# Kernel tuning notes

Measured on AMD Instinct MI355X. Metric: run time of the kernel, lower is better.

Reference implementation:

```python
import jax, jax.numpy as jnp
import numpy as np
from math import sqrt


def setup_inputs() -> dict:
    key = jax.random.key(0)
    ks = jax.random.split(key, 10)
    N, C = 192, 96  # C = N // 2
    n, h, w = 8, 64, 64
    s = lambda fan_in: 1.0 / np.sqrt(fan_in)
    return {
        "x": jax.random.normal(ks[0], (n, N, h, w), dtype=jnp.float32),
        "pe": jax.random.normal(ks[1], (N, 120, 120), dtype=jnp.float32) * 0.02,
        "wq": jax.random.normal(ks[2], (C, N), dtype=jnp.float32) * s(N),
        "bq": jax.random.normal(ks[3], (C,), dtype=jnp.float32) * 0.01,
        "wk": jax.random.normal(ks[4], (C, N), dtype=jnp.float32) * s(N),
        "bk": jax.random.normal(ks[5], (C,), dtype=jnp.float32) * 0.01,
        "wv": jax.random.normal(ks[6], (C, N), dtype=jnp.float32) * s(N),
        "bv": jax.random.normal(ks[7], (C,), dtype=jnp.float32) * 0.01,
        "wz": jax.random.normal(ks[8], (N, C), dtype=jnp.float32) * s(C),
        "bz": jax.random.normal(ks[9], (N,), dtype=jnp.float32) * 0.01,
    }


def _conv1x1(x, w, b):
    # x: [n, cin, h, w]; w: [cout, cin]; b: [cout]
    return jnp.einsum("oc,nchw->nohw", w, x) + b[None, :, None, None]


def reference(x, pe, wq, bq, wk, bk, wv, bv, wz, bz):
    n, c_in, h, w = x.shape
    hw = h * w
    # 2D positional encoding, sliced to the actual spatial size
    x = x + pe[None, :, :h, :w]
    c = wq.shape[0]  # N // 2
    q = _conv1x1(x, wq, bq).reshape(n, c, hw)   # [n, c, hw]
    k = _conv1x1(x, wk, bk).reshape(n, c, hw)   # [n, c, hw]
    v = _conv1x1(x, wv, bv).reshape(n, c, hw)   # [n, c, hw]
    scale = sqrt(hw)
    # logits[n, i, j] = sum_c q[n,c,i] * k[n,c,j]
    logits = jnp.einsum("nci,ncj->nij", q, k) / scale  # [n, hw, hw]
    weights = jax.nn.softmax(logits, axis=-1)
    # z[n, c, i] = sum_j weights[n,i,j] * v[n,c,j]
    z = jnp.einsum("nij,ncj->nci", weights, v).reshape(n, c, h, w)
    z = _conv1x1(z, wz, bz)  # [n, N, h, w]
    return x + z
```

## Files before the change

kernel.cpp:

```cpp
#include <hip/hip_runtime.h>
#include <hip/hip_bf16.h>

#define HW 4096
#define CIN 192
#define CMID 96

typedef __attribute__((ext_vector_type(8))) short bf16x8;
typedef __attribute__((ext_vector_type(4))) float f32x4;
typedef __attribute__((ext_vector_type(16))) float f32x16;
typedef __attribute__((ext_vector_type(4))) unsigned int u32x4;

static __device__ __forceinline__ unsigned short f2bf(float f) {
    union { float f; unsigned int u; } v;
    v.f = f;
    unsigned int r = v.u + 0x7fffu + ((v.u >> 16) & 1u);
    return (unsigned short)(r >> 16);
}
static __device__ __forceinline__ float b2f(unsigned short h) {
    union { unsigned int u; float f; } v;
    v.u = ((unsigned int)h) << 16;
    return v.f;
}

static __device__ __forceinline__ void gload16(const void* g, void* l) {
    __builtin_amdgcn_global_load_lds(
        (const __attribute__((address_space(1))) unsigned int*)g,
        (__attribute__((address_space(3))) unsigned int*)l, 16, 0, 0);
}

#define SCQ (0.015625f * 1.44269504089f)

__global__ __launch_bounds__(256) void convw_kernel(
    const float* __restrict__ wq, const float* __restrict__ wk,
    const float* __restrict__ wv, const float* __restrict__ wz,
    unsigned short* __restrict__ wqkvb, unsigned short* __restrict__ wzb)
{
    int idx = blockIdx.x * 256 + threadIdx.x;
    if (idx < 3 * CMID * CIN) {
        int m = idx / (CMID * CIN), r = idx % (CMID * CIN);
        const float* w = (m == 0) ? wq : ((m == 1) ? wk : wv);
        wqkvb[idx] = f2bf(w[r]);
    } else if (idx < 3 * CMID * CIN + CIN * CMID) {
        int r = idx - 3 * CMID * CIN;
        wzb[r] = f2bf(wz[r]);
    }
}

__global__ __launch_bounds__(256) void qkv_kernel(
    const float* __restrict__ x, const float* __restrict__ pe,
    const unsigned short* __restrict__ wqkvb,
    const float* __restrict__ bq, const float* __restrict__ bk,
    const float* __restrict__ bv,
    unsigned short* __restrict__ Q, unsigned short* __restrict__ K,
    unsigned short* __restrict__ V)
{
    const int n = blockIdx.y, i0 = blockIdx.x * 64, t = threadIdx.x;
    __shared__ unsigned short xt[64 * 200];

    for (int idx = t; idx < CIN * 64; idx += 256) {
        int c = idx >> 6, il = idx & 63;
        float v = x[((size_t)n * CIN + c) * HW + i0 + il]
                + pe[c * 14400 + blockIdx.x * 120 + il];
        xt[il * 200 + c] = f2bf(v);
    }
    __syncthreads();

    const int w = t >> 6, lane = t & 63, l15 = lane & 15, lg = lane >> 4;
    const int p0 = w * 16;

    bf16x8 af[6];
    #pragma unroll
    for (int f = 0; f < 6; ++f)
        af[f] = *(const bf16x8*)(xt + (p0 + l15) * 200 + f * 32 + lg * 8);

    #pragma unroll
    for (int ct = 0; ct < 18; ++ct) {
        const int m = ct / 6, c6 = ct % 6;
        f32x4 acc = (f32x4){0.f, 0.f, 0.f, 0.f};
        const unsigned short* wrow = wqkvb + (ct * 16 + l15) * CIN + lg * 8;
        #pragma unroll
        for (int f = 0; f < 6; ++f) {
            bf16x8 wf = *(const bf16x8*)(wrow + f * 32);
            if (m < 2)
                acc = __builtin_amdgcn_mfma_f32_16x16x32_bf16(wf, af[f], acc, 0, 0, 0);
            else
                acc = __builtin_amdgcn_mfma_f32_16x16x32_bf16(af[f], wf, acc, 0, 0, 0);
        }
        if (m < 2) {
            f32x4 bv4 = *(const f32x4*)(((m == 0) ? bq : bk) + c6 * 16 + lg * 4);
            ushort4 pk4;
            if (m == 0) {
                pk4.x = f2bf((acc[0] + bv4[0]) * SCQ);
                pk4.y = f2bf((acc[1] + bv4[1]) * SCQ);
                pk4.z = f2bf((acc[2] + bv4[2]) * SCQ);
                pk4.w = f2bf((acc[3] + bv4[3]) * SCQ);
            } else {
                pk4.x = f2bf(acc[0] + bv4[0]);
                pk4.y = f2bf(acc[1] + bv4[1]);
                pk4.z = f2bf(acc[2] + bv4[2]);
                pk4.w = f2bf(acc[3] + bv4[3]);
            }
            unsigned short* dst = ((m == 0) ? Q : K) + (size_t)n * HW * CMID;
            *(ushort4*)(dst + (size_t)(i0 + p0 + l15) * CMID + c6 * 16 + lg * 4) = pk4;
        } else {
            const float bias = bv[c6 * 16 + l15];
            ushort4 pk4;
            pk4.x = f2bf(acc[0] + bias); pk4.y = f2bf(acc[1] + bias);
            pk4.z = f2bf(acc[2] + bias); pk4.w = f2bf(acc[3] + bias);
            *(ushort4*)(V + (size_t)n * CMID * HW + (size_t)(c6 * 16 + l15) * HW
                          + i0 + p0 + lg * 4) = pk4;
        }
    }
}

__global__ __launch_bounds__(256, 2) void attn_kernel(
    const unsigned short* __restrict__ Q, const unsigned short* __restrict__ K,
    const unsigned short* __restrict__ V,
    unsigned short* __restrict__ zp, float* __restrict__ lp)
{
    const int bid = blockIdx.x;
    const int n    = bid & 7;
    const int iblk = (bid >> 3) & 15;
    const int js   = bid >> 7;

    const int t = threadIdx.x, w = t >> 6, lane = t & 63;
    const int l31 = lane & 31, hi = lane >> 5;
    const int ib = iblk * 256 + w * 64;

    __shared__ unsigned short Ks[3][32 * 128];
    __shared__ unsigned short Vs[2][96 * 64];

    const unsigned short* Qb = Q + (size_t)n * HW * CMID;
    const unsigned short* Kb = K + (size_t)n * HW * CMID;
    const unsigned short* Vb = V + (size_t)n * CMID * HW;

    bf16x8 qf[2][6];
    #pragma unroll
    for (int is = 0; is < 2; ++is)
        #pragma unroll
        for (int kc = 0; kc < 6; ++kc)
            qf[is][kc] = *(const bf16x8*)(Qb + (size_t)(ib + is * 32 + l31) * CMID
                                            + kc * 16 + hi * 8);

    int ksoff[2], vsoff[3];
    #pragma unroll
    for (int s = 0; s < 2; ++s) {
        int row = 8 * w + 4 * s + (lane >> 4);
        ksoff[s] = row * CMID + (((lane & 15) ^ (row & 7)) * 8);
    }
    #pragma unroll
    for (int s = 0; s < 3; ++s) {
        int c = 8 * (w * 3 + s) + (lane >> 3);
        vsoff[s] = c * HW + (((lane & 7) ^ (c & 7)) * 8);
    }

    const int j00 = js * 1024;

#define STAGE_K(TILE, KB) do {                                                 \
    _Pragma("unroll") for (int s = 0; s < 2; ++s)                              \
        gload16(Kb + (size_t)(j00 + (TILE) * 32) * CMID + ksoff[s],            \
                &Ks[KB][(w * 2 + s) * 512]);                                   \
} while (0)
#define STAGE_V(WND, VB) do {                                                  \
    _Pragma("unroll") for (int s = 0; s < 3; ++s)                              \
        gload16(Vb + (size_t)(j00 + (WND) * 64) + vsoff[s],                    \
                &Vs[VB][(w * 3 + s) * 512]);                                   \
} while (0)

    f32x16 O[2][3];
    #pragma unroll
    for (int is = 0; is < 2; ++is)
        #pragma unroll
        for (int cc = 0; cc < 3; ++cc)
            #pragma unroll
            for (int e = 0; e < 16; ++e) O[is][cc][e] = 0.f;
    float lsum0 = 0.f, lsum1 = 0.f;

    STAGE_K(0, 0);
    STAGE_K(1, 1);
    STAGE_V(0, 0);
    asm volatile("s_waitcnt vmcnt(0)" ::: "memory");
    __builtin_amdgcn_s_barrier();

#define BODY(KBUF, VBUF, VHALF) do {                                           \
    const unsigned short* Kc = &Ks[KBUF][0];                                   \
    const unsigned short* Vc = &Vs[VBUF][0];                                   \
    f32x16 s0, s1;                                                             \
    _Pragma("unroll") for (int e = 0; e < 16; ++e) { s0[e] = 0.f; s1[e] = 0.f; } \
    __builtin_amdgcn_s_setprio(1);                                             \
    _Pragma("unroll") for (int kc = 0; kc < 6; ++kc) {                         \
        bf16x8 kf = *(const bf16x8*)(Kc + l31 * 128 +                          \
                      (((kc * 2 + hi) ^ (l31 & 7)) << 3));                     \
        s0 = __builtin_amdgcn_mfma_f32_32x32x16_bf16(kf, qf[0][kc], s0, 0, 0, 0); \
        s1 = __builtin_amdgcn_mfma_f32_32x32x16_bf16(kf, qf[1][kc], s1, 0, 0, 0); \
    }                                                                          \
    __builtin_amdgcn_s_setprio(0);                                             \
    unsigned pkk[2][4][2];                                                     \
    _Pragma("unroll") for (int q = 0; q < 4; ++q)                              \
        _Pragma("unroll") for (int rp = 0; rp < 2; ++rp) {                     \
            float lo0 = __builtin_exp2f(s0[q * 4 + 2 * rp]);                   \
            float hh0 = __builtin_exp2f(s0[q * 4 + 2 * rp + 1]);               \
            float lo1 = __builtin_exp2f(s1[q * 4 + 2 * rp]);                   \
            float hh1 = __builtin_exp2f(s1[q * 4 + 2 * rp + 1]);               \
            lsum0 += lo0 + hh0; lsum1 += lo1 + hh1;                            \
            asm("v_cvt_pk_bf16_f32 %0, %1, %2"                                 \
                : "=v"(pkk[0][q][rp]) : "v"(lo0), "v"(hh0));                   \
            asm("v_cvt_pk_bf16_f32 %0, %1, %2"                                 \
                : "=v"(pkk[1][q][rp]) : "v"(lo1), "v"(hh1));                   \
        }                                                                      \
    u32x4 pfu[2][2];                                                           \
    _Pragma("unroll") for (int is = 0; is < 2; ++is)                           \
        _Pragma("unroll") for (int jc = 0; jc < 2; ++jc) {                     \
            unsigned x0 = pkk[is][2 * jc][0], y0 = pkk[is][2 * jc + 1][0];     \
            unsigned x1 = pkk[is][2 * jc][1], y1 = pkk[is][2 * jc + 1][1];     \
            asm("v_permlane32_swap_b32 %0, %1" : "+v"(y0), "+v"(x0));          \
            asm("v_permlane32_swap_b32 %0, %1" : "+v"(y1), "+v"(x1));          \
            pfu[is][jc][0] = x0; pfu[is][jc][1] = x1;                          \
            pfu[is][jc][2] = y0; pfu[is][jc][3] = y1;                          \
        }                                                                      \
    __builtin_amdgcn_s_setprio(1);                                             \
    _Pragma("unroll") for (int jc = 0; jc < 2; ++jc) {                         \
        bf16x8 pa0 = __builtin_bit_cast(bf16x8, pfu[0][jc]);                   \
        bf16x8 pa1 = __builtin_bit_cast(bf16x8, pfu[1][jc]);                   \
        _Pragma("unroll") for (int cc = 0; cc < 3; ++cc) {                     \
            bf16x8 vf = *(const bf16x8*)(Vc + (cc * 32 + l31) * 64 +           \
                          ((((VHALF) * 4 + jc * 2 + hi) ^ (l31 & 7)) << 3));   \
            O[0][cc] = __builtin_amdgcn_mfma_f32_32x32x16_bf16(pa0, vf, O[0][cc], 0, 0, 0); \
            O[1][cc] = __builtin_amdgcn_mfma_f32_32x32x16_bf16(pa1, vf, O[1][cc], 0, 0, 0); \
        }                                                                      \
    }                                                                          \
    __builtin_amdgcn_s_setprio(0);                                             \
} while (0)

    int kb = 0, kb1 = 1, kb2 = 2;
    for (int tt = 0; tt < 32; tt += 2) {
        {
            const int pfk = (tt + 2 < 32) ? tt + 2 : 31;
            STAGE_K(pfk, kb2);
            const int wn = (tt >> 1) + 1;
            const int pfw = (wn < 16) ? wn : 15;
            STAGE_V(pfw, wn & 1);
            BODY(kb, (tt >> 1) & 1, 0);
            asm volatile("s_waitcnt vmcnt(5)" ::: "memory");
            __builtin_amdgcn_s_barrier();
        }
        {
            const int pfk = (tt + 3 < 32) ? tt + 3 : 31;
            STAGE_K(pfk, kb);
            BODY(kb1, (tt >> 1) & 1, 1);
            asm volatile("s_waitcnt vmcnt(2)" ::: "memory");
            __builtin_amdgcn_s_barrier();
        }
        const int tmp = kb;
        kb = kb2; kb2 = kb1; kb1 = tmp;
    }
#undef BODY
#undef STAGE_K
#undef STAGE_V

    asm volatile("s_waitcnt vmcnt(0)" ::: "memory");

    unsigned short* zb = zp + ((size_t)js * 8 + n) * HW * CMID;
    #pragma unroll
    for (int is = 0; is < 2; ++is)
        #pragma unroll
        for (int cc = 0; cc < 3; ++cc)
            #pragma unroll
            for (int r = 0; r < 16; ++r) {
                int i = ib + is * 32 + (r & 3) + 8 * (r >> 2) + 4 * hi;
                zb[(size_t)i * CMID + cc * 32 + l31] = f2bf(O[is][cc][r]);
            }

    lsum0 += __shfl_xor(lsum0, 32, 64);
    lsum1 += __shfl_xor(lsum1, 32, 64);
    if (hi == 0) {
        float* lb = lp + ((size_t)js * 8 + n) * HW;
        lb[ib + l31]      = lsum0;
        lb[ib + 32 + l31] = lsum1;
    }
}

__global__ __launch_bounds__(256) void zproj_kernel(
    const unsigned short* __restrict__ zp, const float* __restrict__ lp,
    const unsigned short* __restrict__ wzb, const float* __restrict__ bz,
    const float* __restrict__ x, const float* __restrict__ pe,
    float* __restrict__ out)
{
    const int n = blockIdx.y, i0 = blockIdx.x * 64, t = threadIdx.x;
    __shared__ unsigned short zt[64 * 104];
    __shared__ float ll[64];

    if (t < 64) {
        float s = 0.f;
        #pragma unroll
        for (int sl = 0; sl < 4; ++sl)
            s += lp[(size_t)sl * 8 * HW + (size_t)n * HW + i0 + t];
        ll[t] = 1.f / s;
    }
    __syncthreads();

    for (int idx = t; idx < 64 * 24; idx += 256) {
        int i = idx / 24, c4 = (idx % 24) * 4;
        size_t gidx = ((size_t)n * HW + i0 + i) * CMID + c4;
        float a0 = 0.f, a1 = 0.f, a2 = 0.f, a3 = 0.f;
        #pragma unroll
        for (int sl = 0; sl < 4; ++sl) {
            ushort4 a = *(const ushort4*)(zp + (size_t)sl * 8 * HW * CMID + gidx);
            a0 += b2f(a.x); a1 += b2f(a.y); a2 += b2f(a.z); a3 += b2f(a.w);
        }
        float li = ll[i];
        zt[i * 104 + c4 + 0] = f2bf(a0 * li);
        zt[i * 104 + c4 + 1] = f2bf(a1 * li);
        zt[i * 104 + c4 + 2] = f2bf(a2 * li);
        zt[i * 104 + c4 + 3] = f2bf(a3 * li);
    }
    __syncthreads();

    const int w = t >> 6, lane = t & 63, l15 = lane & 15, lg = lane >> 4;
    const int p0 = w * 16;

    bf16x8 af[3];
    #pragma unroll
    for (int f = 0; f < 3; ++f)
        af[f] = *(const bf16x8*)(zt + (p0 + l15) * 104 + f * 32 + lg * 8);

    #pragma unroll
    for (int ct = 0; ct < 12; ++ct) {
        f32x4 acc = (f32x4){0.f, 0.f, 0.f, 0.f};
        const unsigned short* wrow = wzb + (ct * 16 + l15) * CMID + lg * 8;
        #pragma unroll
        for (int f = 0; f < 3; ++f) {
            bf16x8 wf = *(const bf16x8*)(wrow + f * 32);
            acc = __builtin_amdgcn_mfma_f32_16x16x32_bf16(af[f], wf, acc, 0, 0, 0);
        }
        const int co = ct * 16 + l15;
        const int ibase = i0 + p0 + lg * 4;
        size_t xa = ((size_t)n * CIN + co) * HW + ibase;
        f32x4 xv = *(const f32x4*)(x + xa);
        f32x4 pv = *(const f32x4*)(pe + co * 14400 + blockIdx.x * 120 + p0 + lg * 4);
        const float bias = bz[co];
        f32x4 o;
        #pragma unroll
        for (int r = 0; r < 4; ++r) o[r] = xv[r] + pv[r] + acc[r] + bias;
        *(f32x4*)(out + xa) = o;
    }
}

extern "C" void kernel_launch(void* const* d_in, const int* in_sizes, int n_in,
                              void* d_out, int out_size, void* d_ws, size_t ws_size,
                              hipStream_t stream) {
    const float* x  = (const float*)d_in[0];
    const float* pe = (const float*)d_in[1];
    const float* wq = (const float*)d_in[2];
    const float* bq = (const float*)d_in[3];
    const float* wk = (const float*)d_in[4];
    const float* bk = (const float*)d_in[5];
    const float* wv = (const float*)d_in[6];
    const float* bv = (const float*)d_in[7];
    const float* wz = (const float*)d_in[8];
    const float* bz = (const float*)d_in[9];
    float* out = (float*)d_out;

    char* ws = (char*)d_ws;
    unsigned short* wqkvb = (unsigned short*)(ws);
    unsigned short* wzb   = (unsigned short*)(ws + 131072);
    unsigned short* Qb    = (unsigned short*)(ws + 196608);
    unsigned short* Kb    = (unsigned short*)(ws + 6488064);
    unsigned short* Vb    = (unsigned short*)(ws + 12779520);
    unsigned short* zpb   = (unsigned short*)(ws + 19070976);
    float*          lpb   = (float*)(ws + 44236800);

    convw_kernel<<<288, 256, 0, stream>>>(wq, wk, wv, wz, wqkvb, wzb);
    qkv_kernel<<<dim3(64, 8), 256, 0, stream>>>(x, pe, wqkvb, bq, bk, bv,
                                                Qb, Kb, Vb);
    attn_kernel<<<512, 256, 0, stream>>>(Qb, Kb, Vb, zpb, lpb);
    zproj_kernel<<<dim3(64, 8), 256, 0, stream>>>(zpb, lpb, wzb, bz, x, pe, out);
}
```

Baseline: 124.6 us.

## Split attention keys into more slices, widen QKV blocks, vectorize staging loads

When the workspace is large enough, the attention kernel splits the key dimension into 8 slices of 512 instead of 4 of 1024, doubling the grid to 1024 blocks to improve CU fill. The occupancy hint rises to 3 blocks per CU. The QKV projection now uses 512-thread blocks that split the output tiles across two wave groups, and loads x/pe with float4 plus packed bf16 conversion. The z-projection reduction reads 8 bf16 values per load and writes packed bf16. The trade-off is more partial-sum traffic and reduction work in zproj, plus possible register pressure from the higher occupancy target.

Result: slower. 262.0 us (+110.2%).

```diff
diff --git a/kernel.cpp b/kernel.cpp
--- a/kernel.cpp
+++ b/kernel.cpp
@@ -15,11 +15,6 @@
     v.f = f;
     unsigned int r = v.u + 0x7fffu + ((v.u >> 16) & 1u);
     return (unsigned short)(r >> 16);
-}
-static __device__ __forceinline__ float b2f(unsigned short h) {
-    union { unsigned int u; float f; } v;
-    v.u = ((unsigned int)h) << 16;
-    return v.f;
 }
 
 static __device__ __forceinline__ void gload16(const void* g, void* l) {
@@ -46,7 +41,7 @@
     }
 }
 
-__global__ __launch_bounds__(256) void qkv_kernel(
+__global__ __launch_bounds__(512) void qkv_kernel(
     const float* __restrict__ x, const float* __restrict__ pe,
     const unsigned short* __restrict__ wqkvb,
     const float* __restrict__ bq, const float* __restrict__ bk,
@@ -54,19 +49,30 @@
     unsigned short* __restrict__ Q, unsigned short* __restrict__ K,
     unsigned short* __restrict__ V)
 {
-    const int n = blockIdx.y, i0 = blockIdx.x * 64, t = threadIdx.x;
+    const int n = blockIdx.y, bx = blockIdx.x, i0 = bx * 64, t = threadIdx.x;
     __shared__ unsigned short xt[64 * 200];
 
-    for (int idx = t; idx < CIN * 64; idx += 256) {
-        int c = idx >> 6, il = idx & 63;
-        float v = x[((size_t)n * CIN + c) * HW + i0 + il]
-                + pe[c * 14400 + blockIdx.x * 120 + il];
-        xt[il * 200 + c] = f2bf(v);
+    #pragma unroll
+    for (int it = 0; it < 6; ++it) {
+        int q = t + it * 512;
+        int c = q >> 4, il4 = (q & 15) << 2;
+        f32x4 xv = *(const f32x4*)(x + ((size_t)n * CIN + c) * HW + i0 + il4);
+        f32x4 pv = *(const f32x4*)(pe + c * 14400 + bx * 120 + il4);
+        float a0 = xv[0] + pv[0], a1 = xv[1] + pv[1];
+        float a2 = xv[2] + pv[2], a3 = xv[3] + pv[3];
+        unsigned w01, w23;
+        asm("v_cvt_pk_bf16_f32 %0, %1, %2" : "=v"(w01) : "v"(a0), "v"(a1));
+        asm("v_cvt_pk_bf16_f32 %0, %1, %2" : "=v"(w23) : "v"(a2), "v"(a3));
+        xt[(il4 + 0) * 200 + c] = (unsigned short)w01;
+        xt[(il4 + 1) * 200 + c] = (unsigned short)(w01 >> 16);
+        xt[(il4 + 2) * 200 + c] = (unsigned short)w23;
+        xt[(il4 + 3) * 200 + c] = (unsigned short)(w23 >> 16);
     }
     __syncthreads();
 
     const int w = t >> 6, lane = t & 63, l15 = lane & 15, lg = lane >> 4;
-    const int p0 = w * 16;
+    const int wg = w >> 2;
+    const int p0 = (w & 3) * 16;
 
     bf16x8 af[6];
     #pragma unroll
@@ -74,7 +80,8 @@
         af[f] = *(const bf16x8*)(xt + (p0 + l15) * 200 + f * 32 + lg * 8);
 
     #pragma unroll
-    for (int ct = 0; ct < 18; ++ct) {
+    for (int cc = 0; cc < 9; ++cc) {
+        const int ct = wg * 9 + cc;
         const int m = ct / 6, c6 = ct % 6;
         f32x4 acc = (f32x4){0.f, 0.f, 0.f, 0.f};
         const unsigned short* wrow = wqkvb + (ct * 16 + l15) * CIN + lg * 8;
@@ -113,10 +120,10 @@
     }
 }
 
-__global__ __launch_bounds__(256, 2) void attn_kernel(
+__global__ __launch_bounds__(256, 3) void attn_kernel(
     const unsigned short* __restrict__ Q, const unsigned short* __restrict__ K,
     const unsigned short* __restrict__ V,
-    unsigned short* __restrict__ zp, float* __restrict__ lp)
+    unsigned short* __restrict__ zp, float* __restrict__ lp, int nt)
 {
     const int bid = blockIdx.x;
     const int n    = bid & 7;
@@ -154,7 +161,7 @@
         vsoff[s] = c * HW + (((lane & 7) ^ (c & 7)) * 8);
     }
 
-    const int j00 = js * 1024;
+    const int j00 = js * nt * 32;
 
 #define STAGE_K(TILE, KB) do {                                                 \
     _Pragma("unroll") for (int s = 0; s < 2; ++s)                              \
@@ -233,19 +240,19 @@
 } while (0)
 
     int kb = 0, kb1 = 1, kb2 = 2;
-    for (int tt = 0; tt < 32; tt += 2) {
+    for (int tt = 0; tt < nt; tt += 2) {
         {
-            const int pfk = (tt + 2 < 32) ? tt + 2 : 31;
+            const int pfk = (tt + 2 < nt) ? tt + 2 : nt - 1;
             STAGE_K(pfk, kb2);
             const int wn = (tt >> 1) + 1;
-            const int pfw = (wn < 16) ? wn : 15;
+            const int pfw = (wn < (nt >> 1)) ? wn : (nt >> 1) - 1;
             STAGE_V(pfw, wn & 1);
             BODY(kb, (tt >> 1) & 1, 0);
             asm volatile("s_waitcnt vmcnt(5)" ::: "memory");
             __builtin_amdgcn_s_barrier();
         }
         {
-            const int pfk = (tt + 3 < 32) ? tt + 3 : 31;
+            const int pfk = (tt + 3 < nt) ? tt + 3 : nt - 1;
             STAGE_K(pfk, kb);
             BODY(kb1, (tt >> 1) & 1, 1);
             asm volatile("s_waitcnt vmcnt(2)" ::: "memory");
@@ -284,7 +291,7 @@
     const unsigned short* __restrict__ zp, const float* __restrict__ lp,
     const unsigned short* __restrict__ wzb, const float* __restrict__ bz,
     const float* __restrict__ x, const float* __restrict__ pe,
-    float* __restrict__ out)
+    float* __restrict__ out, int JS)
 {
     const int n = blockIdx.y, i0 = blockIdx.x * 64, t = threadIdx.x;
     __shared__ unsigned short zt[64 * 104];
@@ -292,27 +299,40 @@
 
     if (t < 64) {
         float s = 0.f;
-        #pragma unroll
-        for (int sl = 0; sl < 4; ++sl)
+        for (int sl = 0; sl < JS; ++sl)
             s += lp[(size_t)sl * 8 * HW + (size_t)n * HW + i0 + t];
         ll[t] = 1.f / s;
     }
     __syncthreads();
 
-    for (int idx = t; idx < 64 * 24; idx += 256) {
-        int i = idx / 24, c4 = (idx % 24) * 4;
-        size_t gidx = ((size_t)n * HW + i0 + i) * CMID + c4;
-        float a0 = 0.f, a1 = 0.f, a2 = 0.f, a3 = 0.f;
-        #pragma unroll
-        for (int sl = 0; sl < 4; ++sl) {
-            ushort4 a = *(const ushort4*)(zp + (size_t)sl * 8 * HW * CMID + gidx);
-            a0 += b2f(a.x); a1 += b2f(a.y); a2 += b2f(a.z); a3 += b2f(a.w);
+    #pragma unroll
+    for (int u = 0; u < 3; ++u) {
+        int unit = t + u * 256;
+        int i = unit / 12, g = unit % 12;
+        size_t gidx = ((size_t)n * HW + i0 + i) * CMID + g * 8;
+        float a[8];
+        #pragma unroll
+        for (int e = 0; e < 8; ++e) a[e] = 0.f;
+        for (int sl = 0; sl < JS; ++sl) {
+            u32x4 wv = *(const u32x4*)(zp + (size_t)sl * 8 * HW * CMID + gidx);
+            #pragma unroll
+            for (int k = 0; k < 4; ++k) {
+                union { unsigned u; float f; } lo, hi2;
+                lo.u = wv[k] << 16;
+                hi2.u = wv[k] & 0xffff0000u;
+                a[2 * k]     += lo.f;
+                a[2 * k + 1] += hi2.f;
+            }
         }
         float li = ll[i];
-        zt[i * 104 + c4 + 0] = f2bf(a0 * li);
-        zt[i * 104 + c4 + 1] = f2bf(a1 * li);
-        zt[i * 104 + c4 + 2] = f2bf(a2 * li);
-        zt[i * 104 + c4 + 3] = f2bf(a3 * li);
+        unsigned ww[4];
+        #pragma unroll
+        for (int k = 0; k < 4; ++k) {
+            float p0 = a[2 * k] * li, p1 = a[2 * k + 1] * li;
+            asm("v_cvt_pk_bf16_f32 %0, %1, %2" : "=v"(ww[k]) : "v"(p0), "v"(p1));
+        }
+        u32x4 wv4 = {ww[0], ww[1], ww[2], ww[3]};
+        *(u32x4*)(zt + i * 104 + g * 8) = wv4;
     }
     __syncthreads();
 
@@ -362,17 +382,22 @@
     float* out = (float*)d_out;
 
     char* ws = (char*)d_ws;
+    const size_t NEED8 = 70451200;
+    const int JS = (ws_size >= NEED8) ? 8 : 4;
+    const int nt = (JS == 8) ? 16 : 32;
+
     unsigned short* wqkvb = (unsigned short*)(ws);
     unsigned short* wzb   = (unsigned short*)(ws + 131072);
     unsigned short* Qb    = (unsigned short*)(ws + 196608);
     unsigned short* Kb    = (unsigned short*)(ws + 6488064);
     unsigned short* Vb    = (unsigned short*)(ws + 12779520);
     unsigned short* zpb   = (unsigned short*)(ws + 19070976);
-    float*          lpb   = (float*)(ws + 44236800);
+    float*          lpb   = (float*)(ws + 19070976 + (size_t)JS * 6291456);
 
     convw_kernel<<<288, 256, 0, stream>>>(wq, wk, wv, wz, wqkvb, wzb);
-    qkv_kernel<<<dim3(64, 8), 256, 0, stream>>>(x, pe, wqkvb, bq, bk, bv,
+    qkv_kernel<<<dim3(64, 8), 512, 0, stream>>>(x, pe, wqkvb, bq, bk, bv,
                                                 Qb, Kb, Vb);
-    attn_kernel<<<512, 256, 0, stream>>>(Qb, Kb, Vb, zpb, lpb);
-    zproj_kernel<<<dim3(64, 8), 256, 0, stream>>>(zpb, lpb, wzb, bz, x, pe, out);
-}
+    attn_kernel<<<128 * JS, 256, 0, stream>>>(Qb, Kb, Vb, zpb, lpb, nt);
+    zproj_kernel<<<dim3(64, 8), 256, 0, stream>>>(zpb, lpb, wzb, bz, x, pe,
+                                                  out, JS);
+}
```
